# Performance work log

Measured on AMD Instinct MI355X. Metric: run time of the kernel, lower is better.

## Reference

```python
import jax, jax.numpy as jnp
import numpy as np

N_QUBITS = 10
INPUT_DIM = 49
ENC_LAMBDA = float(np.pi)
ENC_BETA_MAX = 1.0
BATCH = 2048
LOGIT_SCALE_MIN, LOGIT_SCALE_MAX = 0.5, 80.0
LOGIT_CLAMP = 30.0

# arch_mat rows: [control, target, op, axis, feature]; op: ENC=1, ROT=2, CNOT=3; 1-indexed, 0=none.
def _build_arch_mat():
    cols = []
    for b in range(3):
        for q in range(N_QUBITS):  # encoding RY gates
            cols.append((0, q + 1, 1, 2, (b * N_QUBITS + q) % INPUT_DIM + 1))
        for q in range(N_QUBITS):  # trainable RX gates
            cols.append((0, q + 1, 2, 1, 0))
        for q in range(N_QUBITS - 1):  # CNOT chain
            cols.append((q + 1, q + 2, 3, 0, 0))
    return np.asarray(cols, dtype=np.int64).T  # (5, L)

ARCH_MAT = _build_arch_mat()
N_THETA = int(((ARCH_MAT[2] == 2) & (ARCH_MAT[1] > 0) & (ARCH_MAT[3] > 0)).sum())


def _apply_rot(state, ax, q, theta):
    # state: (B, 2,...,2) complex64; theta: scalar or (B,)
    st = jnp.moveaxis(state, 1 + q, -1)
    half = 0.5 * theta
    c, s = jnp.cos(half), jnp.sin(half)
    if c.ndim == 1:  # per-sample angle -> broadcast over remaining qubit axes
        shape = (-1,) + (1,) * (st.ndim - 2)
        c, s = c.reshape(shape), s.reshape(shape)
    s0, s1 = st[..., 0], st[..., 1]
    if ax == 1:  # RX
        n0 = c * s0 - 1j * s * s1
        n1 = c * s1 - 1j * s * s0
    elif ax == 2:  # RY
        n0 = c * s0 - s * s1
        n1 = c * s1 + s * s0
    else:  # RZ
        n0 = (c - 1j * s) * s0
        n1 = (c + 1j * s) * s1
    return jnp.moveaxis(jnp.stack([n0, n1], axis=-1), -1, 1 + q)


def _apply_cnot(state, cq, tq):
    st = jnp.moveaxis(state, (1 + cq, 1 + tq), (-2, -1))
    st = jnp.stack([st[..., 0, :], st[..., 1, ::-1]], axis=-2)
    return jnp.moveaxis(st, (-2, -1), (1 + cq, 1 + tq))


def _circuit(x, theta, enc_alpha_raw, enc_beta_raw):
    B = x.shape[0]
    state = jnp.zeros((B,) + (2,) * N_QUBITS, jnp.complex64)
    state = state.at[(slice(None),) + (0,) * N_QUBITS].set(1.0)
    alpha = jax.nn.softplus(enc_alpha_raw) + 1e-6  # (D,)
    beta = jnp.tanh(enc_beta_raw) * ENC_BETA_MAX   # (D,)
    rot_idx = 0
    for l in range(ARCH_MAT.shape[1]):  # static structural loop over gates
        c, t, op, ax, f1 = (int(v) for v in ARCH_MAT[:, l])
        if op == 1 and t > 0 and ax > 0 and f1 > 0:
            fi = f1 - 1
            ang = ENC_LAMBDA * (alpha[fi] * x[:, fi] + beta[fi])  # (B,)
            state = _apply_rot(state, ax, t - 1, ang)
        elif op == 2 and t > 0 and ax > 0:
            state = _apply_rot(state, ax, t - 1, theta[rot_idx])
            rot_idx += 1
        elif op == 3 and c > 0 and t > 0 and c != t:
            state = _apply_cnot(state, c - 1, t - 1)
    probs = state.real ** 2 + state.imag ** 2  # (B, 2,...,2)
    exps = []
    for q in range(N_QUBITS):  # <Z_q> = p(q=0) - p(q=1)
        p = jnp.moveaxis(probs, 1 + q, -1).reshape(B, -1, 2).sum(axis=1)
        exps.append(p[:, 0] - p[:, 1])
    return jnp.stack(exps, axis=1)  # (B, n_qubits)


def setup_inputs() -> dict:
    key = jax.random.key(0)
    k = jax.random.split(key, 4)
    x = jax.random.normal(k[0], (BATCH, INPUT_DIM), jnp.float32)
    theta = jnp.clip(0.01 * jax.random.normal(k[1], (N_THETA,), jnp.float32), -0.1, 0.1)
    a0 = float(np.log(np.exp(1.0) - 1.0))  # softplus^-1(enc_alpha_init=1.0)
    enc_alpha_raw = jnp.full((INPUT_DIM,), a0, jnp.float32)
    enc_beta_raw = jnp.zeros((INPUT_DIM,), jnp.float32)  # arctanh(0)=0
    head_w = 0.02 * jax.random.normal(k[2], (1, N_QUBITS), jnp.float32)
    bound = 1.0 / float(np.sqrt(N_QUBITS))
    head_b = jax.random.uniform(k[3], (1,), jnp.float32, -bound, bound)
    logit_scale = jnp.asarray(1.0, jnp.float32)
    return {"x": x, "theta": theta, "enc_alpha_raw": enc_alpha_raw, "enc_beta_raw": enc_beta_raw,
            "head_w": head_w, "head_b": head_b, "logit_scale": logit_scale}


def reference(x, theta, enc_alpha_raw, enc_beta_raw, head_w, head_b, logit_scale):
    exps = _circuit(x, theta, enc_alpha_raw, enc_beta_raw)  # (B, n_qubits)
    raw = exps @ head_w.T + head_b                          # (B, 1)
    scale = jnp.clip(logit_scale, LOGIT_SCALE_MIN, LOGIT_SCALE_MAX)
    return jnp.clip(scale * raw, -LOGIT_CLAMP, LOGIT_CLAMP)
```

## Files before the change

kernel.cpp:

```cpp
#include <hip/hip_runtime.h>
#include <math.h>


#define PI_F 3.14159265358979323846f

typedef unsigned v2u __attribute__((ext_vector_type(2)));

#if defined(__has_builtin)
#if __has_builtin(__builtin_amdgcn_permlane16_swap)
#define HAVE_PL16 1
#endif
#if __has_builtin(__builtin_amdgcn_permlane32_swap)
#define HAVE_PL32 1
#endif
#endif

__device__ __forceinline__ float rdlane(float v, int l) {
    return __int_as_float(__builtin_amdgcn_readlane(__float_as_int(v), l));
}

__device__ __forceinline__ float xor1p(float v) {
    return __int_as_float(__builtin_amdgcn_update_dpp(
        0, __float_as_int(v), 0xB1, 0xF, 0xF, true));
}
__device__ __forceinline__ float xor2p(float v) {
    return __int_as_float(__builtin_amdgcn_update_dpp(
        0, __float_as_int(v), 0x4E, 0xF, 0xF, true));
}
__device__ __forceinline__ float xor4p(float v) {
    int t = __builtin_amdgcn_update_dpp(0, __float_as_int(v), 0x1B, 0xF, 0xF, true);
    t = __builtin_amdgcn_update_dpp(0, t, 0x141, 0xF, 0xF, true);
    return __int_as_float(t);
}
__device__ __forceinline__ float xor8p(float v) {
    return __int_as_float(__builtin_amdgcn_update_dpp(
        0, __float_as_int(v), 0x128, 0xF, 0xF, true));
}
__device__ __forceinline__ float xor16p(float v, bool hi) {
#ifdef HAVE_PL16
    v2u r = __builtin_amdgcn_permlane16_swap(
        (unsigned)__float_as_int(v), (unsigned)__float_as_int(v), false, false);
    return __int_as_float((int)(hi ? r.x : r.y));
#else
    return __shfl_xor(v, 16);
#endif
}
__device__ __forceinline__ float xor32p(float v, bool hi) {
#ifdef HAVE_PL32
    v2u r = __builtin_amdgcn_permlane32_swap(
        (unsigned)__float_as_int(v), (unsigned)__float_as_int(v), false, false);
    return __int_as_float((int)(hi ? r.x : r.y));
#else
    return __shfl_xor(v, 32);
#endif
}

template<int Q>
__device__ __forceinline__ float lane_xor(float v, bool hi) {
    if constexpr (Q == 0) return xor1p(v);
    else if constexpr (Q == 1) return xor2p(v);
    else if constexpr (Q == 2) return xor4p(v);
    else if constexpr (Q == 3) return xor8p(v);
    else if constexpr (Q == 4) return xor16p(v, hi);
    else return xor32p(v, hi);
}

template<bool NEG>
__device__ __forceinline__ float2 cgate(const float2 ar2, const float2 ai2,
                                        const float2 br2, const float2 bi2,
                                        const float2 v, const float2 w) {
    float2 acc;
    asm("v_pk_mul_f32 %0, %1, %2" : "=v"(acc) : "v"(ar2), "v"(v));
    if constexpr (!NEG) {
        asm("v_pk_fma_f32 %0, %1, %2, %0 op_sel:[0,1,0] op_sel_hi:[1,0,1] neg_lo:[0,1,0]"
            : "+v"(acc) : "v"(ai2), "v"(v));
        asm("v_pk_fma_f32 %0, %1, %2, %0" : "+v"(acc) : "v"(br2), "v"(w));
    } else {
        asm("v_pk_fma_f32 %0, %1, %2, %0 op_sel:[0,1,0] op_sel_hi:[1,0,1] neg_lo:[1,1,0] neg_hi:[1,0,0]"
            : "+v"(acc) : "v"(ai2), "v"(v));
        asm("v_pk_fma_f32 %0, %1, %2, %0 neg_lo:[1,0,0] neg_hi:[1,0,0]"
            : "+v"(acc) : "v"(br2), "v"(w));
    }
    asm("v_pk_fma_f32 %0, %1, %2, %0 op_sel:[0,1,0] op_sel_hi:[1,0,1] neg_lo:[0,1,0]"
        : "+v"(acc) : "v"(bi2), "v"(w));
    return acc;
}

template<int Q>
__device__ __forceinline__ void lane_gate(float2 (&st)[16], int lane,
                                          float ar, float ai, float br, float bi) {
    const bool hi = (lane & (1 << Q)) != 0;
    const float aiL = hi ? -ai : ai;
    const float brL = hi ? -br : br;
    const float2 ar2 = make_float2(ar, ar);
    const float2 ai2 = make_float2(aiL, aiL);
    const float2 br2 = make_float2(brL, brL);
    const float2 bi2 = make_float2(bi, bi);
    #pragma unroll
    for (int r = 0; r < 16; ++r) {
        float2 p;
        p.x = lane_xor<Q>(st[r].x, hi);
        p.y = lane_xor<Q>(st[r].y, hi);
        st[r] = cgate<false>(ar2, ai2, br2, bi2, st[r], p);
    }
}

template<int RB>
__device__ __forceinline__ void reg_gate(float2 (&st)[16],
                                         float ar, float ai, float br, float bi) {
    const float2 ar2 = make_float2(ar, ar);
    const float2 ai2 = make_float2(ai, ai);
    const float2 br2 = make_float2(br, br);
    const float2 bi2 = make_float2(bi, bi);
    #pragma unroll
    for (int r = 0; r < 16; ++r) {
        if ((r & RB) == 0) {
            const int r1 = r | RB;
            const float2 v0 = st[r], v1 = st[r1];
            st[r]  = cgate<false>(ar2, ai2, br2, bi2, v0, v1);
            st[r1] = cgate<true >(ar2, ai2, br2, bi2, v1, v0);
        }
    }
}

__device__ __forceinline__ void cnot_chain(float2 (&st)[16], int lane) {
    const int srcLane = lane ^ ((lane & 31) << 1);
    float2 t[16];
    #pragma unroll
    for (int r = 0; r < 16; ++r) {
        t[r].x = __shfl(st[r].x, srcLane);
        t[r].y = __shfl(st[r].y, srcLane);
    }
    const bool b5 = (lane & 32) != 0;
    #pragma unroll
    for (int r = 0; r < 16; ++r) {
        const int q0 = r ^ ((r & 7) << 1);
        const int q1 = q0 ^ 1;
        st[r] = b5 ? t[q1] : t[q0];
    }
}

__global__ __launch_bounds__(256, 1) void cqv_kernel(
    const float* __restrict__ x,
    const float* __restrict__ theta,
    const float* __restrict__ alpha_raw,
    const float* __restrict__ beta_raw,
    const float* __restrict__ head_w,
    const float* __restrict__ head_b,
    const float* __restrict__ logit_scale,
    float* __restrict__ out,
    int batch)
{
    const int lane = threadIdx.x & 63;
    const int wave = threadIdx.x >> 6;
    const int s = blockIdx.x * (blockDim.x >> 6) + wave;
    if (s >= batch) return;

    const int g = (lane < 30) ? lane : 0;
    const float alpha = log1pf(__expf(alpha_raw[g])) + 1e-6f;
    const float beta  = tanhf(beta_raw[g]);
    const float halfE = 0.5f * PI_F * (alpha * x[s * 49 + g] + beta);
    float cE, sE, cT, sT;
    __sincosf(halfE, &sE, &cE);
    __sincosf(0.5f * theta[g], &sT, &cT);

    float2 st[16];

    {
        float u0r[10], u0i[10], u1r[10], u1i[10];
        #pragma unroll
        for (int q = 0; q < 10; ++q) {
            const float ce = rdlane(cE, q), se = rdlane(sE, q);
            const float ct = rdlane(cT, q), s_t = rdlane(sT, q);
            u0r[q] = ct * ce;  u0i[q] = -s_t * se;
            u1r[q] = ct * se;  u1i[q] = -s_t * ce;
        }
        float plr = 1.f, pli = 0.f;
        #pragma unroll
        for (int q = 0; q < 6; ++q) {
            const bool bq = (lane >> q) & 1;
            const float wr = bq ? u1r[q] : u0r[q];
            const float wi = bq ? u1i[q] : u0i[q];
            const float nr = plr * wr - pli * wi;
            const float ni = plr * wi + pli * wr;
            plr = nr; pli = ni;
        }
        float t67r[4], t67i[4], t89r[4], t89i[4];
        #pragma unroll
        for (int a = 0; a < 4; ++a) {
            const float w6r = (a & 1) ? u1r[6] : u0r[6], w6i = (a & 1) ? u1i[6] : u0i[6];
            const float w7r = (a & 2) ? u1r[7] : u0r[7], w7i = (a & 2) ? u1i[7] : u0i[7];
            t67r[a] = w6r * w7r - w6i * w7i;  t67i[a] = w6r * w7i + w6i * w7r;
            const float w8r = (a & 1) ? u1r[8] : u0r[8], w8i = (a & 1) ? u1i[8] : u0i[8];
            const float w9r = (a & 2) ? u1r[9] : u0r[9], w9i = (a & 2) ? u1i[9] : u0i[9];
            t89r[a] = w8r * w9r - w8i * w9i;  t89i[a] = w8r * w9i + w8i * w9r;
        }
        #pragma unroll
        for (int r = 0; r < 16; ++r) {
            const float ar = t67r[r & 3] * t89r[r >> 2] - t67i[r & 3] * t89i[r >> 2];
            const float ai = t67r[r & 3] * t89i[r >> 2] + t67i[r & 3] * t89r[r >> 2];
            st[r].x = ar * plr - ai * pli;
            st[r].y = ar * pli + ai * plr;
        }
    }
    cnot_chain(st, lane);

    #pragma unroll 1
    for (int b = 1; b < 3; ++b) {
        const int base = b * 10;
#define GATE_PARAMS(Q) \
        const float ce = rdlane(cE, base + (Q)), se = rdlane(sE, base + (Q)); \
        const float ct = rdlane(cT, base + (Q)), s_t = rdlane(sT, base + (Q));
#define APPLY_LANE_GATE(Q) { GATE_PARAMS(Q) \
        lane_gate<Q>(st, lane, ct * ce, -s_t * se, -ct * se, -s_t * ce); }
#define APPLY_REG_GATE(Q, RB) { GATE_PARAMS(Q) \
        reg_gate<RB>(st, ct * ce, -s_t * se, -ct * se, -s_t * ce); }
        APPLY_LANE_GATE(0)
        APPLY_LANE_GATE(1)
        APPLY_LANE_GATE(2)
        APPLY_LANE_GATE(3)
        APPLY_LANE_GATE(4)
        APPLY_LANE_GATE(5)
        APPLY_REG_GATE(6, 1)
        APPLY_REG_GATE(7, 2)
        APPLY_REG_GATE(8, 4)
        APPLY_REG_GATE(9, 8)
#undef GATE_PARAMS
#undef APPLY_LANE_GATE
#undef APPLY_REG_GATE
        cnot_chain(st, lane);
    }

    float w[10];
    #pragma unroll
    for (int q = 0; q < 10; ++q) w[q] = head_w[q];
    float wlane = 0.f;
    #pragma unroll
    for (int q = 0; q < 6; ++q) wlane += ((lane >> q) & 1) ? -w[q] : w[q];
    float acc = 0.f, psum = 0.f;
    #pragma unroll
    for (int r = 0; r < 16; ++r) {
        const float p = st[r].x * st[r].x + st[r].y * st[r].y;
        const float wr = ((r & 1) ? -w[6] : w[6]) + ((r & 2) ? -w[7] : w[7])
                       + ((r & 4) ? -w[8] : w[8]) + ((r & 8) ? -w[9] : w[9]);
        psum += p;
        acc = fmaf(wr, p, acc);
    }
    float partial = fmaf(wlane, psum, acc);
    #pragma unroll
    for (int off = 32; off >= 1; off >>= 1) partial += __shfl_xor(partial, off);

    if (lane == 0) {
        const float scale = fminf(fmaxf(logit_scale[0], 0.5f), 80.f);
        const float raw = partial + head_b[0];
        out[s] = fminf(fmaxf(scale * raw, -30.f), 30.f);
    }
}

extern "C" void kernel_launch(void* const* d_in, const int* in_sizes, int n_in,
                              void* d_out, int out_size, void* d_ws, size_t ws_size,
                              hipStream_t stream) {
    const int B = in_sizes[0] / 49;
    const int WPB = 4;
    dim3 block(64 * WPB);
    dim3 grid((B + WPB - 1) / WPB);
    cqv_kernel<<<grid, block, 0, stream>>>(
        (const float*)d_in[0], (const float*)d_in[1], (const float*)d_in[2],
        (const float*)d_in[3], (const float*)d_in[4], (const float*)d_in[5],
        (const float*)d_in[6], (float*)d_out, B);
}
```

Measured before the change: 84.71 us.

## Split each sample's state vector across two waves with LDS exchange for qubit 9

Each sample's 1024-amplitude state is now spread over two wavefronts of 8 registers per lane, not one wave of 16. Qubit 9 becomes a cross-wave bit, so its gate and the CNOT permutation go through double-buffered LDS with block-wide barriers, and the final reduction combines the two wave partials via shared memory. Launch bounds are raised to allow more resident blocks. The aim is to halve per-wave register pressure and work, raising occupancy and parallelism, at the cost of LDS traffic and __syncthreads stalls.

```diff
diff --git a/kernel.cpp b/kernel.cpp
--- a/kernel.cpp
+++ b/kernel.cpp
@@ -87,7 +87,7 @@
 }
 
 template<int Q>
-__device__ __forceinline__ void lane_gate(float2 (&st)[16], int lane,
+__device__ __forceinline__ void lane_gate(float2 (&st)[8], int lane,
                                           float ar, float ai, float br, float bi) {
     const bool hi = (lane & (1 << Q)) != 0;
     const float aiL = hi ? -ai : ai;
@@ -97,7 +97,7 @@
     const float2 br2 = make_float2(brL, brL);
     const float2 bi2 = make_float2(bi, bi);
     #pragma unroll
-    for (int r = 0; r < 16; ++r) {
+    for (int r = 0; r < 8; ++r) {
         float2 p;
         p.x = lane_xor<Q>(st[r].x, hi);
         p.y = lane_xor<Q>(st[r].y, hi);
@@ -106,14 +106,14 @@
 }
 
 template<int RB>
-__device__ __forceinline__ void reg_gate(float2 (&st)[16],
+__device__ __forceinline__ void reg_gate(float2 (&st)[8],
                                          float ar, float ai, float br, float bi) {
     const float2 ar2 = make_float2(ar, ar);
     const float2 ai2 = make_float2(ai, ai);
     const float2 br2 = make_float2(br, br);
     const float2 bi2 = make_float2(bi, bi);
     #pragma unroll
-    for (int r = 0; r < 16; ++r) {
+    for (int r = 0; r < 8; ++r) {
         if ((r & RB) == 0) {
             const int r1 = r | RB;
             const float2 v0 = st[r], v1 = st[r1];
@@ -123,24 +123,7 @@
     }
 }
 
-__device__ __forceinline__ void cnot_chain(float2 (&st)[16], int lane) {
-    const int srcLane = lane ^ ((lane & 31) << 1);
-    float2 t[16];
-    #pragma unroll
-    for (int r = 0; r < 16; ++r) {
-        t[r].x = __shfl(st[r].x, srcLane);
-        t[r].y = __shfl(st[r].y, srcLane);
-    }
-    const bool b5 = (lane & 32) != 0;
-    #pragma unroll
-    for (int r = 0; r < 16; ++r) {
-        const int q0 = r ^ ((r & 7) << 1);
-        const int q1 = q0 ^ 1;
-        st[r] = b5 ? t[q1] : t[q0];
-    }
-}
-
-__global__ __launch_bounds__(256, 1) void cqv_kernel(
+__global__ __launch_bounds__(256, 4) void cqv_kernel(
     const float* __restrict__ x,
     const float* __restrict__ theta,
     const float* __restrict__ alpha_raw,
@@ -152,9 +135,17 @@
     int batch)
 {
     const int lane = threadIdx.x & 63;
-    const int wave = threadIdx.x >> 6;
-    const int s = blockIdx.x * (blockDim.x >> 6) + wave;
+    const int wavid = threadIdx.x >> 6;
+    const int p  = wavid >> 1;
+    const int wv = wavid & 1;
+    const int s = blockIdx.x * 2 + p;
     if (s >= batch) return;
+
+    __shared__ float2 lds[2][2][8][2][64];
+    __shared__ float pbuf[2][2];
+
+    const int l5 = (lane >> 5) & 1;
+    const int srcLane = lane ^ ((lane & 31) << 1);
 
     const int g = (lane < 30) ? lane : 0;
     const float alpha = log1pf(__expf(alpha_raw[g])) + 1e-6f;
@@ -164,7 +155,7 @@
     __sincosf(halfE, &sE, &cE);
     __sincosf(0.5f * theta[g], &sT, &cT);
 
-    float2 st[16];
+    float2 st[8];
 
     {
         float u0r[10], u0i[10], u1r[10], u1i[10];
@@ -185,25 +176,39 @@
             const float ni = plr * wi + pli * wr;
             plr = nr; pli = ni;
         }
-        float t67r[4], t67i[4], t89r[4], t89i[4];
+        const float w9r = wv ? u1r[9] : u0r[9], w9i = wv ? u1i[9] : u0i[9];
+        float t67r[4], t67i[4], t89r[2], t89i[2];
         #pragma unroll
         for (int a = 0; a < 4; ++a) {
             const float w6r = (a & 1) ? u1r[6] : u0r[6], w6i = (a & 1) ? u1i[6] : u0i[6];
             const float w7r = (a & 2) ? u1r[7] : u0r[7], w7i = (a & 2) ? u1i[7] : u0i[7];
             t67r[a] = w6r * w7r - w6i * w7i;  t67i[a] = w6r * w7i + w6i * w7r;
-            const float w8r = (a & 1) ? u1r[8] : u0r[8], w8i = (a & 1) ? u1i[8] : u0i[8];
-            const float w9r = (a & 2) ? u1r[9] : u0r[9], w9i = (a & 2) ? u1i[9] : u0i[9];
-            t89r[a] = w8r * w9r - w8i * w9i;  t89i[a] = w8r * w9i + w8i * w9r;
-        }
-        #pragma unroll
-        for (int r = 0; r < 16; ++r) {
+        }
+        #pragma unroll
+        for (int k = 0; k < 2; ++k) {
+            const float w8r = k ? u1r[8] : u0r[8], w8i = k ? u1i[8] : u0i[8];
+            t89r[k] = w8r * w9r - w8i * w9i;  t89i[k] = w8r * w9i + w8i * w9r;
+        }
+        #pragma unroll
+        for (int r = 0; r < 8; ++r) {
             const float ar = t67r[r & 3] * t89r[r >> 2] - t67i[r & 3] * t89i[r >> 2];
             const float ai = t67r[r & 3] * t89i[r >> 2] + t67i[r & 3] * t89r[r >> 2];
             st[r].x = ar * plr - ai * pli;
             st[r].y = ar * pli + ai * plr;
         }
     }
-    cnot_chain(st, lane);
+
+    {
+        #pragma unroll
+        for (int r = 0; r < 8; ++r) lds[0][p][r][wv][lane] = st[r];
+        __syncthreads();
+        #pragma unroll
+        for (int r = 0; r < 8; ++r) {
+            const int sReg = (r ^ ((r & 3) << 1)) ^ l5;
+            const int k9 = wv ^ (r >> 2);
+            st[r] = lds[0][p][sReg][k9][srcLane];
+        }
+    }
 
     #pragma unroll 1
     for (int b = 1; b < 3; ++b) {
@@ -224,35 +229,53 @@
         APPLY_REG_GATE(6, 1)
         APPLY_REG_GATE(7, 2)
         APPLY_REG_GATE(8, 4)
-        APPLY_REG_GATE(9, 8)
+
+        const int db = b & 1;
+        GATE_PARAMS(9)
+        const float ar = ct * ce, ai = -s_t * se, br = -ct * se, bi = -s_t * ce;
+        const float2 ar2 = make_float2(ar, ar), ai2 = make_float2(ai, ai);
+        const float2 br2 = make_float2(br, br), bi2 = make_float2(bi, bi);
+        #pragma unroll
+        for (int r = 0; r < 8; ++r) lds[db][p][r][wv][lane] = st[r];
+        __syncthreads();
+        #pragma unroll
+        for (int r = 0; r < 8; ++r) {
+            const int sReg = (r ^ ((r & 3) << 1)) ^ l5;
+            const int k9 = wv ^ (r >> 2);
+            const float2 v = lds[db][p][sReg][k9][srcLane];
+            const float2 w = lds[db][p][sReg][k9 ^ 1][srcLane];
+            if (k9 == 0) st[r] = cgate<false>(ar2, ai2, br2, bi2, v, w);
+            else         st[r] = cgate<true >(ar2, ai2, br2, bi2, v, w);
+        }
 #undef GATE_PARAMS
 #undef APPLY_LANE_GATE
 #undef APPLY_REG_GATE
-        cnot_chain(st, lane);
     }
 
     float w[10];
     #pragma unroll
     for (int q = 0; q < 10; ++q) w[q] = head_w[q];
-    float wlane = 0.f;
+    float wlane = wv ? -w[9] : w[9];
     #pragma unroll
     for (int q = 0; q < 6; ++q) wlane += ((lane >> q) & 1) ? -w[q] : w[q];
     float acc = 0.f, psum = 0.f;
     #pragma unroll
-    for (int r = 0; r < 16; ++r) {
-        const float p = st[r].x * st[r].x + st[r].y * st[r].y;
+    for (int r = 0; r < 8; ++r) {
+        const float pw = st[r].x * st[r].x + st[r].y * st[r].y;
         const float wr = ((r & 1) ? -w[6] : w[6]) + ((r & 2) ? -w[7] : w[7])
-                       + ((r & 4) ? -w[8] : w[8]) + ((r & 8) ? -w[9] : w[9]);
-        psum += p;
-        acc = fmaf(wr, p, acc);
+                       + ((r & 4) ? -w[8] : w[8]);
+        psum += pw;
+        acc = fmaf(wr, pw, acc);
     }
     float partial = fmaf(wlane, psum, acc);
     #pragma unroll
     for (int off = 32; off >= 1; off >>= 1) partial += __shfl_xor(partial, off);
 
-    if (lane == 0) {
+    if (lane == 0) pbuf[p][wv] = partial;
+    __syncthreads();
+    if (lane == 0 && wv == 0) {
         const float scale = fminf(fmaxf(logit_scale[0], 0.5f), 80.f);
-        const float raw = partial + head_b[0];
+        const float raw = pbuf[p][0] + pbuf[p][1] + head_b[0];
         out[s] = fminf(fmaxf(scale * raw, -30.f), 30.f);
     }
 }
@@ -261,9 +284,8 @@
                               void* d_out, int out_size, void* d_ws, size_t ws_size,
                               hipStream_t stream) {
     const int B = in_sizes[0] / 49;
-    const int WPB = 4;
-    dim3 block(64 * WPB);
-    dim3 grid((B + WPB - 1) / WPB);
+    dim3 block(256);
+    dim3 grid((B + 1) / 2);
     cqv_kernel<<<grid, block, 0, stream>>>(
         (const float*)d_in[0], (const float*)d_in[1], (const float*)d_in[2],
         (const float*)d_in[3], (const float*)d_in[4], (const float*)d_in[5],
```

Result: faster. 81.23 us (-4.1%).
